# Performance work log

Hardware: AMD Instinct MI355X
Metric: run time of the kernel (lower is better)

Reference implementation:

```python
import jax, jax.numpy as jnp
import numpy as np

BT = 64  # chunk size

def _l2norm(x, eps=1e-6):
    n = jnp.linalg.norm(x, axis=-1, keepdims=True)
    return x / jnp.maximum(n, eps)

def _kda_gate(g_raw, A_log, dt_bias):
    # g = -exp(A_log) * softplus(g_raw + dt_bias); broadcast A_log over K
    return -jnp.exp(A_log)[None, None, :, None] * jax.nn.softplus(g_raw.astype(jnp.float32) + dt_bias[None, None].astype(jnp.float32))

def _chunk_kda_fwd(q, k, v, g, beta):
    B, T, H, K = q.shape
    V = v.shape[-1]
    assert T % BT == 0
    NT = T // BT
    scale = K ** -0.5
    q = _l2norm(q.astype(jnp.float32)) * scale
    k = _l2norm(k.astype(jnp.float32))

    def to_chunks(x, d):
        # [B,T,H,d] -> [NT,B,H,BT,d]
        return x.astype(jnp.float32).transpose(0, 2, 1, 3).reshape(B, H, NT, BT, d).transpose(2, 0, 1, 3, 4)

    qc, kc, vc, gc = to_chunks(q, K), to_chunks(k, K), to_chunks(v, V), to_chunks(g, K)
    bc = beta.astype(jnp.float32).transpose(0, 2, 1).reshape(B, H, NT, BT).transpose(2, 0, 1, 3)  # [NT,B,H,BT]

    eye = jnp.eye(BT, dtype=jnp.float32)
    tril_strict = jnp.tril(jnp.ones((BT, BT), bool), -1)
    tril_incl = jnp.tril(jnp.ones((BT, BT), bool), 0)

    def body(S, xs):
        q_i, k_i, v_i, g_i, b_i = xs  # [B,H,BT,*]
        gcum = jnp.cumsum(g_i, axis=-2)                              # [B,H,BT,K]
        diff = gcum[:, :, :, None, :] - gcum[:, :, None, :, :]      # [B,H,BT,BT,K]
        decay = jnp.exp(jnp.minimum(diff, 0.0))
        # intra-chunk k-k matrix, beta row-scaled, strictly lower, negated
        Akk = jnp.einsum('bhik,bhjk,bhijk->bhij', k_i, k_i, decay)
        M = -jnp.where(tril_strict, Akk * b_i[..., :, None], 0.0)
        # UT transform: torch in-place loop solves Tm = (I - M)^{-1}
        Tm = jax.scipy.linalg.solve_triangular(eye - M, jnp.broadcast_to(eye, M.shape), lower=True)
        Afin = Tm * b_i[..., None, :]                                # column scale by beta
        k_eg = k_i * jnp.exp(gcum)
        w = Afin @ k_eg                                              # [B,H,BT,K]
        u = Afin @ v_i                                               # [B,H,BT,V]
        Aqk = jnp.einsum('bhik,bhjk,bhijk->bhij', q_i, k_i, decay)
        Aqk = jnp.where(tril_incl, Aqk, 0.0)
        v_new = u - w @ S
        o_i = (q_i * jnp.exp(gcum)) @ S + Aqk @ v_new
        g_last = gcum[:, :, -1, :]                                   # [B,H,K]
        k_dec = jnp.exp(g_last[:, :, None, :] - gcum) * k_i
        S_new = S * jnp.exp(g_last)[..., None] + jnp.einsum('bhck,bhcv->bhkv', k_dec, v_new)
        return S_new, o_i

    S0 = jnp.zeros((B, H, K, V), jnp.float32)
    _, o = jax.lax.scan(body, S0, (qc, kc, vc, gc, bc))              # o: [NT,B,H,BT,V]
    return o.transpose(1, 2, 0, 3, 4).reshape(B, H, T, V).transpose(0, 2, 1, 3)


def setup_inputs() -> dict:
    key = jax.random.key(0)
    ks = jax.random.split(key, 7)
    B, T, H, K, V = 2, 8192, 16, 32, 64
    return {
        'q': jax.random.normal(ks[0], (B, T, H, K), jnp.float32),
        'k': jax.random.normal(ks[1], (B, T, H, K), jnp.float32),
        'v': jax.random.normal(ks[2], (B, T, H, V), jnp.float32),
        'g_raw': jax.random.normal(ks[3], (B, T, H, K), jnp.float32),
        'beta': jax.random.uniform(ks[4], (B, T, H), jnp.float32),
        'A_log': jax.random.normal(ks[5], (H,), jnp.float32) - 3.0,  # moderate decay rate
        'dt_bias': jax.random.normal(ks[6], (H, K), jnp.float32) * 0.1,
    }


def reference(q, k, v, g_raw, beta, A_log, dt_bias):
    g = _kda_gate(g_raw, A_log, dt_bias)
    return _chunk_kda_fwd(q, k, v, g, beta)
```

## Files before the change

### kernel.cpp

```cpp
#include <hip/hip_runtime.h>
#include <math.h>

#define Tt 8192
#define Hh 16
#define NCH 4096

#define OFF_U   ((size_t)NCH*2048)
#define OFF_M   ((size_t)NCH*6144)
#define OFF_C   ((size_t)NCH*7168)
#define OFF_MS  ((size_t)NCH*9216)
#define OFF_CS  (OFF_MS + (size_t)256*1024)
#define OFF_SS  (OFF_CS + (size_t)256*2048)

__device__ __forceinline__ float softplusf(float x) {
  return fmaxf(x, 0.f) + log1pf(__expf(-fabsf(x)));
}


__global__ __launch_bounds__(256) void kda_phase1(
    const float* __restrict__ kin, const float* __restrict__ vin,
    const float* __restrict__ graw, const float* __restrict__ beta,
    const float* __restrict__ A_log, const float* __restrict__ dt_bias,
    float* __restrict__ ws)
{
  __shared__ float sG[64*33];
  __shared__ float sK[64*33];
  __shared__ float sU[2816];
  __shared__ float sW[3104];

  const int tid = threadIdx.x;
  const int ch = blockIdx.x;
  const int c = ch >> 5, bh = ch & 31;
  const int b = bh >> 4, h = bh & 15;
  const int t0 = c*64;
  const int iq = tid >> 2, kq = (tid & 3)*8;

  float* wsW = ws;
  float* wsU = ws + OFF_U;
  float* wsM = ws + OFF_M;
  float* wsCc= ws + OFF_C;

  const float negA = -__expf(A_log[h]);

  {
    const float* gr = graw + (((size_t)b*Tt + t0 + iq)*Hh + h)*32 + kq;
    const float* db = dt_bias + h*32 + kq;
    #pragma unroll
    for (int r = 0; r < 8; ++r)
      sG[iq*33 + kq + r] = negA * softplusf(gr[r] + db[r]);
  }
  __syncthreads();
  if (tid < 32) {
    float c0 = 0.f;
    for (int blk = 0; blk < 4; ++blk) {
      float v[16];
      #pragma unroll
      for (int i = 0; i < 16; ++i) v[i] = sG[(blk*16+i)*33 + tid];
      #pragma unroll
      for (int i = 0; i < 16; ++i) { c0 += v[i]; sG[(blk*16+i)*33 + tid] = c0; }
    }
  }
  {
    const float* kp = kin + (((size_t)b*Tt + t0 + iq)*Hh + h)*32 + kq;
    float kr[8]; float ss = 0.f;
    #pragma unroll
    for (int r = 0; r < 8; ++r) { kr[r] = kp[r]; ss += kr[r]*kr[r]; }
    ss += __shfl_xor(ss, 1); ss += __shfl_xor(ss, 2);
    const float sc = 1.f / fmaxf(sqrtf(ss), 1e-6f);
    #pragma unroll
    for (int r = 0; r < 8; ++r) sK[iq*33 + kq + r] = kr[r]*sc;
  }
  __syncthreads();

  const float b_cm = beta[((size_t)b*Tt + t0 + (tid & 63))*Hh + h];
  float* P  = sU;
  float* Qb = sU + 2304;
  const int i64 = tid & 63;
  const int w4 = (tid >> 6)*2;
  const int pL = i64 >> 4, pLb = pL*(pL+1)/2, iL = i64 & 15;
  for (int jt = 0; jt < 4; ++jt) {
    const int j0 = jt*16;
    {
      float pv[8];
      #pragma unroll
      for (int r = 0; r < 8; ++r) {
        const int idx = iq*33 + kq + r;
        pv[r] = sK[idx] * __expf(fminf(sG[idx] - sG[j0*33 + kq + r], 0.f));
      }
      *(float4*)(P + iq*36 + kq)     = make_float4(pv[0],pv[1],pv[2],pv[3]);
      *(float4*)(P + iq*36 + kq + 4) = make_float4(pv[4],pv[5],pv[6],pv[7]);
    }
    {
      const int jj = tid >> 4, kk = tid & 15;
      Qb[jj*32 + kk]      = sK[(j0+jj)*33 + kk]      * __expf(sG[j0*33 + kk]      - sG[(j0+jj)*33 + kk]);
      Qb[jj*32 + kk + 16] = sK[(j0+jj)*33 + kk + 16] * __expf(sG[j0*33 + kk + 16] - sG[(j0+jj)*33 + kk + 16]);
    }
    __syncthreads();
    float a0 = 0.f, a1 = 0.f, a2 = 0.f, a3 = 0.f;
    #pragma unroll
    for (int t8 = 0; t8 < 8; ++t8) {
      const int k0 = t8*4;
      const float4 pa = *(const float4*)(P  + i64*36 + k0);
      const float4 xa = *(const float4*)(Qb + (w4  )*32 + k0);
      const float4 xb = *(const float4*)(Qb + (w4+1)*32 + k0);
      const float4 xc = *(const float4*)(Qb + (w4+8)*32 + k0);
      const float4 xd = *(const float4*)(Qb + (w4+9)*32 + k0);
      a0 += pa.x*xa.x + pa.y*xa.y + pa.z*xa.z + pa.w*xa.w;
      a1 += pa.x*xb.x + pa.y*xb.y + pa.z*xb.z + pa.w*xb.w;
      a2 += pa.x*xc.x + pa.y*xc.y + pa.z*xc.z + pa.w*xc.w;
      a3 += pa.x*xd.x + pa.y*xd.y + pa.z*xd.z + pa.w*xd.w;
    }
    if (pL >= jt) {
      float* Lb = sW + (pLb + jt)*256 + iL;
      Lb[(w4  )*16] = (i64 > j0+w4  ) ? a0*b_cm : 0.f;
      Lb[(w4+1)*16] = (i64 > j0+w4+1) ? a1*b_cm : 0.f;
      Lb[(w4+8)*16] = (i64 > j0+w4+8) ? a2*b_cm : 0.f;
      Lb[(w4+9)*16] = (i64 > j0+w4+9) ? a3*b_cm : 0.f;
    }
    __syncthreads();
  }

  if (tid < 64) {
    const int p = tid >> 4, col = tid & 15;
    const int bD = p*(p+1)/2 + p;
    float* Td = sU + bD*272;
    const float* Ld = sW + bD*256;
    Td[col] = (col == 0) ? 1.f : 0.f;
    for (int i = 1; i < 16; ++i) {
      float acc = 0.f;
      for (int j = 0; j < i; ++j)
        acc -= Ld[j*16 + i] * Td[j*17 + col];
      Td[i*17 + col] = acc + ((i == col) ? 1.f : 0.f);
    }
  }
  __syncthreads();
  {
    const int wid = tid >> 6;
    const int lane = tid & 63;
    const int ri = lane & 15, c4 = (lane >> 4)*4;
    float* Ct = sW + 2560 + wid*272;
    auto offblk = [&](int p, int q) {
      const int pb = p*(p+1)/2;
      float a0=0.f, a1=0.f, a2=0.f, a3=0.f;
      for (int m = q; m < p; ++m) {
        const float* Lb = sW + (pb + m)*256;
        const float* Tb = sU + (m*(m+1)/2 + q)*272;
        #pragma unroll
        for (int j = 0; j < 16; ++j) {
          const float lv = Lb[j*16 + ri];
          const float* tp = Tb + j*17 + c4;
          a0 += lv*tp[0]; a1 += lv*tp[1]; a2 += lv*tp[2]; a3 += lv*tp[3];
        }
      }
      float* cp = Ct + ri*17 + c4;
      cp[0]=a0; cp[1]=a1; cp[2]=a2; cp[3]=a3;
      const float* Tpp = sU + (pb + p)*272 + ri*17;
      float b0=0.f, b1=0.f, b2=0.f, b3=0.f;
      #pragma unroll
      for (int j = 0; j < 16; ++j) {
        const float tv = Tpp[j];
        const float* cj = Ct + j*17 + c4;
        b0 += tv*cj[0]; b1 += tv*cj[1]; b2 += tv*cj[2]; b3 += tv*cj[3];
      }
      float* op = sU + (pb + q)*272 + ri*17 + c4;
      op[0]=-b0; op[1]=-b1; op[2]=-b2; op[3]=-b3;
    };
    if (wid == 0) offblk(1,0); else if (wid == 1) offblk(2,1);
    __syncthreads();
    if (wid == 0) offblk(2,0); else if (wid == 1) offblk(3,1);
    __syncthreads();
    if (wid == 0) offblk(3,0); else if (wid == 1) offblk(3,2);
  }
  __syncthreads();

  {
    const float b_row = beta[((size_t)b*Tt + t0 + iq)*Hh + h];
    #pragma unroll
    for (int r = 0; r < 8; ++r) {
      const int idx = iq*33 + kq + r;
      const float g = sG[idx], kn = sK[idx];
      sW[iq*32 + kq + r] = b_row * kn * __expf(g);
      sK[idx] = kn * __expf(sG[63*33 + kq + r] - g);
    }
    if (tid < 32) sW[3072 + tid] = __expf(sG[63*33 + tid]);
  }
  __syncthreads();

  const int pT = iq >> 4, pTb = pT*(pT+1)/2;
  const int r17 = (iq & 15)*17, iqm = iq & 15;

  {
    float acc[8] = {0,0,0,0,0,0,0,0};
    for (int m = 0; m <= pT; ++m) {
      const float* Tb = sU + (pTb + m)*272 + r17;
      const int jmax = (m == pT) ? iqm : 15;
      const float* eb = sW + m*16*32 + kq;
      for (int jj = 0; jj <= jmax; ++jj) {
        const float t = Tb[jj];
        const float4 e0 = *(const float4*)(eb + jj*32);
        const float4 e1 = *(const float4*)(eb + jj*32 + 4);
        acc[0]+=t*e0.x; acc[1]+=t*e0.y; acc[2]+=t*e0.z; acc[3]+=t*e0.w;
        acc[4]+=t*e1.x; acc[5]+=t*e1.y; acc[6]+=t*e1.z; acc[7]+=t*e1.w;
      }
    }
    #pragma unroll
    for (int r = 0; r < 8; ++r) {
      wsW[(size_t)ch*2048 + tid*8 + r] = acc[r];
      sG[iq*32 + kq + r] = acc[r];
    }
  }
  __syncthreads();

  const int vs8 = (tid & 3)*8;
  for (int vh = 0; vh < 2; ++vh) {
    {
      #pragma unroll
      for (int r = 0; r < 2; ++r) {
        const int f = tid + 256*r;
        const int j = f >> 3, cc = (f & 7)*4;
        const float bj = beta[((size_t)b*Tt + t0 + j)*Hh + h];
        float4 v4 = *(const float4*)(vin + (((size_t)b*Tt + t0 + j)*Hh + h)*64 + vh*32 + cc);
        v4.x *= bj; v4.y *= bj; v4.z *= bj; v4.w *= bj;
        *(float4*)(sW + j*32 + cc) = v4;
      }
    }
    __syncthreads();
    float ua[8];
    {
      #pragma unroll
      for (int r = 0; r < 8; ++r) ua[r] = 0.f;
      for (int m = 0; m <= pT; ++m) {
        const float* Tb = sU + (pTb + m)*272 + r17;
        const int jmax = (m == pT) ? iqm : 15;
        const float* eb = sW + m*16*32 + vs8;
        for (int jj = 0; jj <= jmax; ++jj) {
          const float t = Tb[jj];
          const float4 e0 = *(const float4*)(eb + jj*32);
          const float4 e1 = *(const float4*)(eb + jj*32 + 4);
          ua[0]+=t*e0.x; ua[1]+=t*e0.y; ua[2]+=t*e0.z; ua[3]+=t*e0.w;
          ua[4]+=t*e1.x; ua[5]+=t*e1.y; ua[6]+=t*e1.z; ua[7]+=t*e1.w;
        }
      }
      *(float4*)(wsU + (size_t)ch*4096 + iq*64 + vh*32 + vs8)     = make_float4(ua[0],ua[1],ua[2],ua[3]);
      *(float4*)(wsU + (size_t)ch*4096 + iq*64 + vh*32 + vs8 + 4) = make_float4(ua[4],ua[5],ua[6],ua[7]);
    }
    __syncthreads();
    *(float4*)(sW + iq*32 + vs8)     = make_float4(ua[0],ua[1],ua[2],ua[3]);
    *(float4*)(sW + iq*32 + vs8 + 4) = make_float4(ua[4],ua[5],ua[6],ua[7]);
    __syncthreads();
    if (vh == 0) {
      const int a = tid >> 3, b4 = (tid & 7)*4;
      float mA[4] = {0.f,0.f,0.f,0.f};
      for (int t = 0; t < 64; ++t) {
        const float kd = sK[t*33 + a];
        const float4 wv = *(const float4*)(sG + t*32 + b4);
        mA[0]+=kd*wv.x; mA[1]+=kd*wv.y; mA[2]+=kd*wv.z; mA[3]+=kd*wv.w;
      }
      const float eg = sW[3072 + a];
      float4 m4;
      m4.x = ((a == b4+0) ? eg : 0.f) - mA[0];
      m4.y = ((a == b4+1) ? eg : 0.f) - mA[1];
      m4.z = ((a == b4+2) ? eg : 0.f) - mA[2];
      m4.w = ((a == b4+3) ? eg : 0.f) - mA[3];
      *(float4*)(wsM + (size_t)ch*1024 + tid*4) = m4;
    }
    {
      const int a = tid >> 3, c4c = (tid & 7)*4;
      float cA[4] = {0.f,0.f,0.f,0.f};
      for (int t = 0; t < 64; ++t) {
        const float kd = sK[t*33 + a];
        const float4 u4 = *(const float4*)(sW + t*32 + c4c);
        cA[0]+=kd*u4.x; cA[1]+=kd*u4.y; cA[2]+=kd*u4.z; cA[3]+=kd*u4.w;
      }
      *(float4*)(wsCc + (size_t)ch*2048 + a*64 + vh*32 + c4c) = make_float4(cA[0],cA[1],cA[2],cA[3]);
    }
    __syncthreads();
  }
}

__global__ __launch_bounds__(256) void kda_scanA(float* __restrict__ ws)
{
  __shared__ float sMa[32*33];
  __shared__ float sMc[32*33];
  __shared__ float sCa[32*18];
  const int tid = threadIdx.x;
  const int vt = blockIdx.x & 3, seg = (blockIdx.x >> 2) & 7, bh = blockIdx.x >> 5;
  const int v0 = vt*16;
  const int a = tid >> 3, b4 = (tid & 7)*4, c2 = (tid & 7)*2;
  const float* wsM = ws + OFF_M;
  const float* wsC = ws + OFF_C;

  #pragma unroll
  for (int r = 0; r < 4; ++r) sMa[a*33 + b4 + r] = (a == b4 + r) ? 1.f : 0.f;
  sCa[a*18 + c2] = 0.f; sCa[a*18 + c2 + 1] = 0.f;

  int ch = (seg*16)*32 + bh;
  float4 m4 = *(const float4*)(wsM + (size_t)ch*1024 + tid*4);
  float2 cc = *(const float2*)(wsC + (size_t)ch*2048 + a*64 + v0 + c2);

  for (int i = 0; i < 16; ++i) {
    sMc[a*33+b4+0]=m4.x; sMc[a*33+b4+1]=m4.y; sMc[a*33+b4+2]=m4.z; sMc[a*33+b4+3]=m4.w;
    __syncthreads();
    float4 m4n = m4; float2 ccn = cc;
    if (i < 15) {
      const int chn = (seg*16 + i + 1)*32 + bh;
      m4n = *(const float4*)(wsM + (size_t)chn*1024 + tid*4);
      ccn = *(const float2*)(wsC + (size_t)chn*2048 + a*64 + v0 + c2);
    }
    float cn0 = cc.x, cn1 = cc.y;
    float mn0=0.f, mn1=0.f, mn2=0.f, mn3=0.f;
    for (int bb = 0; bb < 32; ++bb) {
      const float m = sMc[a*33 + bb];
      const float2 s2 = *(const float2*)(sCa + bb*18 + c2);
      cn0 += m*s2.x; cn1 += m*s2.y;
      mn0 += m*sMa[bb*33+b4+0]; mn1 += m*sMa[bb*33+b4+1];
      mn2 += m*sMa[bb*33+b4+2]; mn3 += m*sMa[bb*33+b4+3];
    }
    __syncthreads();
    sCa[a*18+c2] = cn0; sCa[a*18+c2+1] = cn1;
    sMa[a*33+b4+0]=mn0; sMa[a*33+b4+1]=mn1; sMa[a*33+b4+2]=mn2; sMa[a*33+b4+3]=mn3;
    m4 = m4n; cc = ccn;
  }
  const size_t sid = (size_t)(bh*8 + seg);
  float* wsMs = ws + OFF_MS;
  float* wsCs = ws + OFF_CS;
  if (vt == 0) {
    #pragma unroll
    for (int r = 0; r < 4; ++r) wsMs[sid*1024 + tid*4 + r] = sMa[a*33+b4+r];
  }
  float2 co; co.x = sCa[a*18+c2]; co.y = sCa[a*18+c2+1];
  *(float2*)(wsCs + sid*2048 + a*64 + v0 + c2) = co;
}

__global__ __launch_bounds__(256) void kda_scanB(float* __restrict__ ws)
{
  __shared__ float sS[32*18];
  __shared__ float sM[32*33];
  const int tid = threadIdx.x;
  const int vt = blockIdx.x & 3, bh = blockIdx.x >> 2;
  const int v0 = vt*16;
  const int a = tid >> 3, b4 = (tid & 7)*4, c2 = (tid & 7)*2;
  const float* wsMs = ws + OFF_MS;
  const float* wsCs = ws + OFF_CS;
  float* wsSs = ws + OFF_SS;

  float s0 = 0.f, s1 = 0.f;
  sS[a*18 + c2] = 0.f; sS[a*18 + c2 + 1] = 0.f;
  const size_t sid0 = (size_t)(bh*8);
  float4 m4 = *(const float4*)(wsMs + sid0*1024 + tid*4);
  float2 cc = *(const float2*)(wsCs + sid0*2048 + a*64 + v0 + c2);

  for (int seg = 0; seg < 8; ++seg) {
    const size_t sid = (size_t)(bh*8 + seg);
    *(float2*)(wsSs + sid*2048 + a*64 + v0 + c2) = make_float2(s0, s1);
    sM[a*33+b4+0]=m4.x; sM[a*33+b4+1]=m4.y; sM[a*33+b4+2]=m4.z; sM[a*33+b4+3]=m4.w;
    __syncthreads();
    float4 m4n = m4; float2 ccn = cc;
    if (seg < 7) {
      m4n = *(const float4*)(wsMs + (sid+1)*1024 + tid*4);
      ccn = *(const float2*)(wsCs + (sid+1)*2048 + a*64 + v0 + c2);
    }
    float n0 = cc.x, n1 = cc.y;
    for (int bb = 0; bb < 32; ++bb) {
      const float m = sM[a*33 + bb];
      const float2 s2 = *(const float2*)(sS + bb*18 + c2);
      n0 += m*s2.x; n1 += m*s2.y;
    }
    __syncthreads();
    s0 = n0; s1 = n1;
    sS[a*18+c2] = s0; sS[a*18+c2+1] = s1;
    m4 = m4n; cc = ccn;
  }
}

__global__ __launch_bounds__(256) void kda_scanC(float* __restrict__ ws)
{
  __shared__ float sM[32*33];
  __shared__ float sS[32*18];
  const int tid = threadIdx.x;
  const int vt = blockIdx.x & 3, seg = (blockIdx.x >> 2) & 7, bh = blockIdx.x >> 5;
  const int v0 = vt*16;
  const int a = tid >> 3, b4 = (tid & 7)*4, c2 = (tid & 7)*2;
  const float* wsM = ws + OFF_M;
  float* wsC = ws + OFF_C;
  const float* wsSs = ws + OFF_SS;

  const size_t sid = (size_t)(bh*8 + seg);
  float s0, s1;
  {
    float2 sv = *(const float2*)(wsSs + sid*2048 + a*64 + v0 + c2);
    s0 = sv.x; s1 = sv.y;
    sS[a*18 + c2] = s0; sS[a*18 + c2 + 1] = s1;
  }
  int ch = (seg*16)*32 + bh;
  float4 m4 = *(const float4*)(wsM + (size_t)ch*1024 + tid*4);
  float2 cc = *(const float2*)(wsC + (size_t)ch*2048 + a*64 + v0 + c2);

  for (int i = 0; i < 16; ++i) {
    const int chc = (seg*16 + i)*32 + bh;
    sM[a*33+b4+0]=m4.x; sM[a*33+b4+1]=m4.y; sM[a*33+b4+2]=m4.z; sM[a*33+b4+3]=m4.w;
    *(float2*)(wsC + (size_t)chc*2048 + a*64 + v0 + c2) = make_float2(s0, s1);
    __syncthreads();
    float4 m4n = m4; float2 ccn = cc;
    if (i < 15) {
      const int chn = (seg*16 + i + 1)*32 + bh;
      m4n = *(const float4*)(wsM + (size_t)chn*1024 + tid*4);
      ccn = *(const float2*)(wsC + (size_t)chn*2048 + a*64 + v0 + c2);
    }
    float n0 = cc.x, n1 = cc.y;
    for (int bb = 0; bb < 32; ++bb) {
      const float m = sM[a*33 + bb];
      const float2 s2 = *(const float2*)(sS + bb*18 + c2);
      n0 += m*s2.x; n1 += m*s2.y;
    }
    __syncthreads();
    s0 = n0; s1 = n1;
    sS[a*18+c2] = s0; sS[a*18+c2+1] = s1;
    m4 = m4n; cc = ccn;
  }
}

__global__ __launch_bounds__(256) void kda_phase3(
    const float* __restrict__ qin, const float* __restrict__ kin,
    const float* __restrict__ graw,
    const float* __restrict__ A_log, const float* __restrict__ dt_bias,
    const float* __restrict__ ws, float* __restrict__ out)
{
  __shared__ float sG[64*33];
  __shared__ float sQ[64*33];
  __shared__ float sA[2720];
  __shared__ float sV[2816];

  const int tid = threadIdx.x;
  const int ch = blockIdx.x;
  const int c = ch >> 5, bh = ch & 31;
  const int b = bh >> 4, h = bh & 15;
  const int t0 = c*64;
  const int iq = tid >> 2, kq = (tid & 3)*8;

  const float* wsW = ws;
  const float* wsU = ws + OFF_U;
  const float* wsS = ws + OFF_C;

  const float negA = -__expf(A_log[h]);
  {
    const float* gr = graw + (((size_t)b*Tt + t0 + iq)*Hh + h)*32 + kq;
    const float* db = dt_bias + h*32 + kq;
    #pragma unroll
    for (int r = 0; r < 8; ++r)
      sG[iq*33 + kq + r] = negA * softplusf(gr[r] + db[r]);
  }
  __syncthreads();
  if (tid < 32) {
    float c0 = 0.f;
    for (int blk = 0; blk < 4; ++blk) {
      float v[16];
      #pragma unroll
      for (int i = 0; i < 16; ++i) v[i] = sG[(blk*16+i)*33 + tid];
      #pragma unroll
      for (int i = 0; i < 16; ++i) { c0 += v[i]; sG[(blk*16+i)*33 + tid] = c0; }
    }
  }
  float knr[8];
  {
    const float* qp = qin + (((size_t)b*Tt + t0 + iq)*Hh + h)*32 + kq;
    float qr[8]; float ssq = 0.f;
    #pragma unroll
    for (int r = 0; r < 8; ++r) { qr[r] = qp[r]; ssq += qr[r]*qr[r]; }
    ssq += __shfl_xor(ssq, 1); ssq += __shfl_xor(ssq, 2);
    const float scq = 0.17677669529663687f / fmaxf(sqrtf(ssq), 1e-6f);
    #pragma unroll
    for (int r = 0; r < 8; ++r) sQ[iq*33 + kq + r] = qr[r]*scq;

    const float* kp = kin + (((size_t)b*Tt + t0 + iq)*Hh + h)*32 + kq;
    float ssk = 0.f;
    #pragma unroll
    for (int r = 0; r < 8; ++r) { knr[r] = kp[r]; ssk += knr[r]*knr[r]; }
    ssk += __shfl_xor(ssk, 1); ssk += __shfl_xor(ssk, 2);
    const float sck = 1.f / fmaxf(sqrtf(ssk), 1e-6f);
    #pragma unroll
    for (int r = 0; r < 8; ++r) knr[r] *= sck;
  }
  __syncthreads();

  float* P  = sV;
  float* Qb = sV + 2304;
  const int i64 = tid & 63;
  const int w4 = (tid >> 6)*2;
  const int pL = i64 >> 4, pLb = pL*(pL+1)/2, iL = i64 & 15;
  for (int jt = 0; jt < 4; ++jt) {
    const int j0 = jt*16;
    {
      float pv[8];
      #pragma unroll
      for (int r = 0; r < 8; ++r) {
        const int idx = iq*33 + kq + r;
        pv[r] = sQ[idx] * __expf(fminf(sG[idx] - sG[j0*33 + kq + r], 0.f));
      }
      *(float4*)(P + iq*36 + kq)     = make_float4(pv[0],pv[1],pv[2],pv[3]);
      *(float4*)(P + iq*36 + kq + 4) = make_float4(pv[4],pv[5],pv[6],pv[7]);
    }
    if (iq >= j0 && iq < j0 + 16) {
      const int jj = iq - j0;
      #pragma unroll
      for (int r = 0; r < 8; ++r)
        Qb[jj*32 + kq + r] = knr[r] * __expf(sG[j0*33 + kq + r] - sG[iq*33 + kq + r]);
    }
    __syncthreads();
    float a0 = 0.f, a1 = 0.f, a2 = 0.f, a3 = 0.f;
    #pragma unroll
    for (int t8 = 0; t8 < 8; ++t8) {
      const int k0 = t8*4;
      const float4 pa = *(const float4*)(P  + i64*36 + k0);
      const float4 xa = *(const float4*)(Qb + (w4  )*32 + k0);
      const float4 xb = *(const float4*)(Qb + (w4+1)*32 + k0);
      const float4 xc = *(const float4*)(Qb + (w4+8)*32 + k0);
      const float4 xd = *(const float4*)(Qb + (w4+9)*32 + k0);
      a0 += pa.x*xa.x + pa.y*xa.y + pa.z*xa.z + pa.w*xa.w;
      a1 += pa.x*xb.x + pa.y*xb.y + pa.z*xb.z + pa.w*xb.w;
      a2 += pa.x*xc.x + pa.y*xc.y + pa.z*xc.z + pa.w*xc.w;
      a3 += pa.x*xd.x + pa.y*xd.y + pa.z*xd.z + pa.w*xd.w;
    }
    if (pL >= jt) {
      float* Ab = sA + (pLb + jt)*272 + iL*17;
      Ab[w4  ] = (i64 >= j0+w4  ) ? a0 : 0.f;
      Ab[w4+1] = (i64 >= j0+w4+1) ? a1 : 0.f;
      Ab[w4+8] = (i64 >= j0+w4+8) ? a2 : 0.f;
      Ab[w4+9] = (i64 >= j0+w4+9) ? a3 : 0.f;
    }
    __syncthreads();
  }

  float qgr[8];
  {
    #pragma unroll
    for (int r = 0; r < 8; ++r) {
      const int idx = iq*33 + kq + r;
      qgr[r] = sQ[idx] * __expf(sG[idx]);
    }
  }
  __syncthreads();
  {
    #pragma unroll
    for (int rr = 0; rr < 2; ++rr) {
      const int f = tid + 256*rr;
      *(float4*)(sG + f*4) = *(const float4*)(wsS + (size_t)ch*2048 + f*4);
    }
    *(float4*)(sV + tid*8)     = *(const float4*)(wsW + (size_t)ch*2048 + tid*8);
    *(float4*)(sV + tid*8 + 4) = *(const float4*)(wsW + (size_t)ch*2048 + tid*8 + 4);
  }
  __syncthreads();
  const int pT = iq >> 4, pTb = pT*(pT+1)/2;
  const int r17 = (iq & 15)*17, iqm = iq & 15;
  {
    float qe[8];
    #pragma unroll
    for (int r = 0; r < 8; ++r) qe[r] = qgr[r];
    for (int m = 0; m <= pT; ++m) {
      const float* Ab = sA + (pTb + m)*272 + r17;
      const int jmax = (m == pT) ? iqm : 15;
      const float* wb = sV + m*16*32 + kq;
      for (int jj = 0; jj <= jmax; ++jj) {
        const float av = Ab[jj];
        const float4 w0 = *(const float4*)(wb + jj*32);
        const float4 w1 = *(const float4*)(wb + jj*32 + 4);
        qe[0]-=av*w0.x; qe[1]-=av*w0.y; qe[2]-=av*w0.z; qe[3]-=av*w0.w;
        qe[4]-=av*w1.x; qe[5]-=av*w1.y; qe[6]-=av*w1.z; qe[7]-=av*w1.w;
      }
    }
    #pragma unroll
    for (int r = 0; r < 8; ++r) sQ[iq*33 + kq + r] = qe[r];
  }
  __syncthreads();

  {
    const int vs = (tid & 3)*16;
    float acc[16];
    #pragma unroll
    for (int r = 0; r < 16; ++r) acc[r] = 0.f;
    for (int vh = 0; vh < 2; ++vh) {
      {
        #pragma unroll
        for (int rr = 0; rr < 2; ++rr) {
          const int f = tid + 256*rr;
          *(float4*)(sV + f*4) = *(const float4*)(wsU + (size_t)ch*4096 + vh*2048 + f*4);
        }
      }
      __syncthreads();
      if (vh == 0) {
        for (int kk = 0; kk < 32; ++kk) {
          const float qv = sQ[iq*33 + kk];
          const float4 s0 = *(const float4*)(sG + kk*64 + vs);
          const float4 s1 = *(const float4*)(sG + kk*64 + vs + 4);
          const float4 s2 = *(const float4*)(sG + kk*64 + vs + 8);
          const float4 s3 = *(const float4*)(sG + kk*64 + vs + 12);
          acc[0]+=qv*s0.x;  acc[1]+=qv*s0.y;  acc[2]+=qv*s0.z;  acc[3]+=qv*s0.w;
          acc[4]+=qv*s1.x;  acc[5]+=qv*s1.y;  acc[6]+=qv*s1.z;  acc[7]+=qv*s1.w;
          acc[8]+=qv*s2.x;  acc[9]+=qv*s2.y;  acc[10]+=qv*s2.z; acc[11]+=qv*s2.w;
          acc[12]+=qv*s3.x; acc[13]+=qv*s3.y; acc[14]+=qv*s3.z; acc[15]+=qv*s3.w;
        }
      }
      for (int m = vh*2; m <= pT && m < vh*2 + 2; ++m) {
        const float* Ab = sA + (pTb + m)*272 + r17;
        const int jmax = (m == pT) ? iqm : 15;
        const float* ub = sV + (m - vh*2)*16*64 + vs;
        for (int jj = 0; jj <= jmax; ++jj) {
          const float av = Ab[jj];
          const float4 u0 = *(const float4*)(ub + jj*64);
          const float4 u1 = *(const float4*)(ub + jj*64 + 4);
          const float4 u2 = *(const float4*)(ub + jj*64 + 8);
          const float4 u3 = *(const float4*)(ub + jj*64 + 12);
          acc[0]+=av*u0.x;  acc[1]+=av*u0.y;  acc[2]+=av*u0.z;  acc[3]+=av*u0.w;
          acc[4]+=av*u1.x;  acc[5]+=av*u1.y;  acc[6]+=av*u1.z;  acc[7]+=av*u1.w;
          acc[8]+=av*u2.x;  acc[9]+=av*u2.y;  acc[10]+=av*u2.z; acc[11]+=av*u2.w;
          acc[12]+=av*u3.x; acc[13]+=av*u3.y; acc[14]+=av*u3.z; acc[15]+=av*u3.w;
        }
      }
      if (vh == 0) __syncthreads();
    }
    float* op = out + (((size_t)b*Tt + t0 + iq)*Hh + h)*64 + vs;
    #pragma unroll
    for (int rr = 0; rr < 4; ++rr) {
      float4 o4; o4.x=acc[rr*4]; o4.y=acc[rr*4+1]; o4.z=acc[rr*4+2]; o4.w=acc[rr*4+3];
      *(float4*)(op + rr*4) = o4;
    }
  }
}

extern "C" void kernel_launch(void* const* d_in, const int* in_sizes, int n_in,
                              void* d_out, int out_size, void* d_ws, size_t ws_size,
                              hipStream_t stream) {
  const float* q    = (const float*)d_in[0];
  const float* k    = (const float*)d_in[1];
  const float* v    = (const float*)d_in[2];
  const float* graw = (const float*)d_in[3];
  const float* beta = (const float*)d_in[4];
  const float* A_log= (const float*)d_in[5];
  const float* dtb  = (const float*)d_in[6];
  float* out = (float*)d_out;
  float* ws  = (float*)d_ws;

  kda_phase1<<<NCH, 256, 0, stream>>>(k, v, graw, beta, A_log, dtb, ws);
  kda_scanA<<<1024, 256, 0, stream>>>(ws);
  kda_scanB<<<128, 256, 0, stream>>>(ws);
  kda_scanC<<<1024, 256, 0, stream>>>(ws);
  kda_phase3<<<NCH, 256, 0, stream>>>(q, k, graw, A_log, dtb, ws, out);
}
```

Baseline: 523.9 us.

## Fold segment scan into scanC and prefetch global loads into registers

Removes the separate scanB kernel. Each scanC block now recomputes its segment's starting state by walking the preceding segment summaries itself, which saves a launch and the workspace round trip for the segment states but adds redundant work that grows with segment index. Phase1 and phase3 also issue their v/beta, S, W and U global loads at kernel start into registers, so memory latency overlaps earlier compute. The cost is higher register pressure.

```diff
diff --git a/kernel.cpp b/kernel.cpp
--- a/kernel.cpp
+++ b/kernel.cpp
@@ -10,7 +10,6 @@
 #define OFF_C   ((size_t)NCH*7168)
 #define OFF_MS  ((size_t)NCH*9216)
 #define OFF_CS  (OFF_MS + (size_t)256*1024)
-#define OFF_SS  (OFF_CS + (size_t)256*2048)
 
 __device__ __forceinline__ float softplusf(float x) {
   return fmaxf(x, 0.f) + log1pf(__expf(-fabsf(x)));
@@ -41,6 +40,22 @@
   float* wsCc= ws + OFF_C;
 
   const float negA = -__expf(A_log[h]);
+
+  float4 vpre[2][2];
+  {
+    #pragma unroll
+    for (int r = 0; r < 2; ++r) {
+      const int f = tid + 256*r;
+      const int j = f >> 3, cc = (f & 7)*4;
+      const float bj = beta[((size_t)b*Tt + t0 + j)*Hh + h];
+      const float* vp = vin + (((size_t)b*Tt + t0 + j)*Hh + h)*64 + cc;
+      float4 v0v = *(const float4*)(vp);
+      float4 v1v = *(const float4*)(vp + 32);
+      v0v.x*=bj; v0v.y*=bj; v0v.z*=bj; v0v.w*=bj;
+      v1v.x*=bj; v1v.y*=bj; v1v.z*=bj; v1v.w*=bj;
+      vpre[0][r] = v0v; vpre[1][r] = v1v;
+    }
+  }
 
   {
     const float* gr = graw + (((size_t)b*Tt + t0 + iq)*Hh + h)*32 + kq;
@@ -212,16 +227,14 @@
   __syncthreads();
 
   const int vs8 = (tid & 3)*8;
+  #pragma unroll
   for (int vh = 0; vh < 2; ++vh) {
     {
       #pragma unroll
       for (int r = 0; r < 2; ++r) {
         const int f = tid + 256*r;
         const int j = f >> 3, cc = (f & 7)*4;
-        const float bj = beta[((size_t)b*Tt + t0 + j)*Hh + h];
-        float4 v4 = *(const float4*)(vin + (((size_t)b*Tt + t0 + j)*Hh + h)*64 + vh*32 + cc);
-        v4.x *= bj; v4.y *= bj; v4.z *= bj; v4.w *= bj;
-        *(float4*)(sW + j*32 + cc) = v4;
+        *(float4*)(sW + j*32 + cc) = vpre[vh][r];
       }
     }
     __syncthreads();
@@ -332,47 +345,6 @@
   *(float2*)(wsCs + sid*2048 + a*64 + v0 + c2) = co;
 }
 
-__global__ __launch_bounds__(256) void kda_scanB(float* __restrict__ ws)
-{
-  __shared__ float sS[32*18];
-  __shared__ float sM[32*33];
-  const int tid = threadIdx.x;
-  const int vt = blockIdx.x & 3, bh = blockIdx.x >> 2;
-  const int v0 = vt*16;
-  const int a = tid >> 3, b4 = (tid & 7)*4, c2 = (tid & 7)*2;
-  const float* wsMs = ws + OFF_MS;
-  const float* wsCs = ws + OFF_CS;
-  float* wsSs = ws + OFF_SS;
-
-  float s0 = 0.f, s1 = 0.f;
-  sS[a*18 + c2] = 0.f; sS[a*18 + c2 + 1] = 0.f;
-  const size_t sid0 = (size_t)(bh*8);
-  float4 m4 = *(const float4*)(wsMs + sid0*1024 + tid*4);
-  float2 cc = *(const float2*)(wsCs + sid0*2048 + a*64 + v0 + c2);
-
-  for (int seg = 0; seg < 8; ++seg) {
-    const size_t sid = (size_t)(bh*8 + seg);
-    *(float2*)(wsSs + sid*2048 + a*64 + v0 + c2) = make_float2(s0, s1);
-    sM[a*33+b4+0]=m4.x; sM[a*33+b4+1]=m4.y; sM[a*33+b4+2]=m4.z; sM[a*33+b4+3]=m4.w;
-    __syncthreads();
-    float4 m4n = m4; float2 ccn = cc;
-    if (seg < 7) {
-      m4n = *(const float4*)(wsMs + (sid+1)*1024 + tid*4);
-      ccn = *(const float2*)(wsCs + (sid+1)*2048 + a*64 + v0 + c2);
-    }
-    float n0 = cc.x, n1 = cc.y;
-    for (int bb = 0; bb < 32; ++bb) {
-      const float m = sM[a*33 + bb];
-      const float2 s2 = *(const float2*)(sS + bb*18 + c2);
-      n0 += m*s2.x; n1 += m*s2.y;
-    }
-    __syncthreads();
-    s0 = n0; s1 = n1;
-    sS[a*18+c2] = s0; sS[a*18+c2+1] = s1;
-    m4 = m4n; cc = ccn;
-  }
-}
-
 __global__ __launch_bounds__(256) void kda_scanC(float* __restrict__ ws)
 {
   __shared__ float sM[32*33];
@@ -383,14 +355,26 @@
   const int a = tid >> 3, b4 = (tid & 7)*4, c2 = (tid & 7)*2;
   const float* wsM = ws + OFF_M;
   float* wsC = ws + OFF_C;
-  const float* wsSs = ws + OFF_SS;
-
-  const size_t sid = (size_t)(bh*8 + seg);
-  float s0, s1;
-  {
-    float2 sv = *(const float2*)(wsSs + sid*2048 + a*64 + v0 + c2);
-    s0 = sv.x; s1 = sv.y;
-    sS[a*18 + c2] = s0; sS[a*18 + c2 + 1] = s1;
+  const float* wsMs = ws + OFF_MS;
+  const float* wsCs = ws + OFF_CS;
+
+  float s0 = 0.f, s1 = 0.f;
+  sS[a*18 + c2] = 0.f; sS[a*18 + c2 + 1] = 0.f;
+  for (int j = 0; j < seg; ++j) {
+    const size_t sj = (size_t)(bh*8 + j);
+    float4 m4p = *(const float4*)(wsMs + sj*1024 + tid*4);
+    float2 csp = *(const float2*)(wsCs + sj*2048 + a*64 + v0 + c2);
+    sM[a*33+b4+0]=m4p.x; sM[a*33+b4+1]=m4p.y; sM[a*33+b4+2]=m4p.z; sM[a*33+b4+3]=m4p.w;
+    __syncthreads();
+    float n0 = csp.x, n1 = csp.y;
+    for (int bb = 0; bb < 32; ++bb) {
+      const float m = sM[a*33 + bb];
+      const float2 s2 = *(const float2*)(sS + bb*18 + c2);
+      n0 += m*s2.x; n1 += m*s2.y;
+    }
+    __syncthreads();
+    s0 = n0; s1 = n1;
+    sS[a*18+c2] = s0; sS[a*18+c2+1] = s1;
   }
   int ch = (seg*16)*32 + bh;
   float4 m4 = *(const float4*)(wsM + (size_t)ch*1024 + tid*4);
@@ -441,6 +425,20 @@
   const float* wsW = ws;
   const float* wsU = ws + OFF_U;
   const float* wsS = ws + OFF_C;
+
+  float4 sPre[2], wPre[2], uPre[4];
+  {
+    #pragma unroll
+    for (int rr = 0; rr < 2; ++rr)
+      sPre[rr] = *(const float4*)(wsS + (size_t)ch*2048 + (tid + 256*rr)*4);
+    wPre[0] = *(const float4*)(wsW + (size_t)ch*2048 + tid*8);
+    wPre[1] = *(const float4*)(wsW + (size_t)ch*2048 + tid*8 + 4);
+    #pragma unroll
+    for (int vh = 0; vh < 2; ++vh)
+      #pragma unroll
+      for (int rr = 0; rr < 2; ++rr)
+        uPre[vh*2+rr] = *(const float4*)(wsU + (size_t)ch*4096 + vh*2048 + (tid + 256*rr)*4);
+  }
 
   const float negA = -__expf(A_log[h]);
   {
@@ -544,10 +542,10 @@
     #pragma unroll
     for (int rr = 0; rr < 2; ++rr) {
       const int f = tid + 256*rr;
-      *(float4*)(sG + f*4) = *(const float4*)(wsS + (size_t)ch*2048 + f*4);
-    }
-    *(float4*)(sV + tid*8)     = *(const float4*)(wsW + (size_t)ch*2048 + tid*8);
-    *(float4*)(sV + tid*8 + 4) = *(const float4*)(wsW + (size_t)ch*2048 + tid*8 + 4);
+      *(float4*)(sG + f*4) = sPre[rr];
+    }
+    *(float4*)(sV + tid*8)     = wPre[0];
+    *(float4*)(sV + tid*8 + 4) = wPre[1];
   }
   __syncthreads();
   const int pT = iq >> 4, pTb = pT*(pT+1)/2;
@@ -578,12 +576,13 @@
     float acc[16];
     #pragma unroll
     for (int r = 0; r < 16; ++r) acc[r] = 0.f;
+    #pragma unroll
     for (int vh = 0; vh < 2; ++vh) {
       {
         #pragma unroll
         for (int rr = 0; rr < 2; ++rr) {
           const int f = tid + 256*rr;
-          *(float4*)(sV + f*4) = *(const float4*)(wsU + (size_t)ch*4096 + vh*2048 + f*4);
+          *(float4*)(sV + f*4) = uPre[vh*2+rr];
         }
       }
       __syncthreads();
@@ -642,7 +641,6 @@
 
   kda_phase1<<<NCH, 256, 0, stream>>>(k, v, graw, beta, A_log, dtb, ws);
   kda_scanA<<<1024, 256, 0, stream>>>(ws);
-  kda_scanB<<<128, 256, 0, stream>>>(ws);
   kda_scanC<<<1024, 256, 0, stream>>>(ws);
   kda_phase3<<<NCH, 256, 0, stream>>>(q, k, graw, A_log, dtb, ws, out);
 }
```

New measurement: 612.5 us. 1.17x slower.
